# Kernel optimization log

Measured on AMD Instinct MI355X. Metric: run time of the kernel, lower is better.

Reference implementation:

```python
import jax, jax.numpy as jnp
import numpy as np

N_GROUPS = 1024   # n
L = 128           # keys per group
R = 4             # queries per group (nq[i] == R)
NQ_TOTAL = N_GROUPS * R
D_Q = 256
D_K = 256
D_Z = 256
D_V = 256


def setup_inputs() -> dict:
    key = jax.random.key(0)
    ks = jax.random.split(key, 8)
    nq = jnp.full((N_GROUPS,), R, dtype=jnp.int32)
    q = jax.random.normal(ks[0], (NQ_TOTAL, D_Q), dtype=jnp.float32)
    k = jax.random.normal(ks[1], (N_GROUPS, L, D_K), dtype=jnp.float32)
    v = jax.random.normal(ks[2], (N_GROUPS, L, D_V), dtype=jnp.float32)
    m = jax.random.uniform(ks[3], (N_GROUPS, L)) < 0.9
    m = m.at[:, 0].set(True)  # guarantee each row has at least one valid key
    Wq = jax.random.normal(ks[4], (D_Q, D_Z), dtype=jnp.float32) / np.sqrt(D_Q)
    bq = jnp.zeros((D_Z,), dtype=jnp.float32)
    Wk = jax.random.normal(ks[5], (D_K, D_Z), dtype=jnp.float32) / np.sqrt(D_K)
    bk = jnp.zeros((D_Z,), dtype=jnp.float32)
    return {"nq": nq, "q": q, "k": k, "v": v, "m": m,
            "Wq": Wq, "bq": bq, "Wk": Wk, "bk": bk}


def reference(nq, q, v, k, m, Wq, bq, Wk, bk):
    # Linear projections (nn.Linear with bias)
    qz = q @ Wq + bq                      # (N, d_z)
    kz = k @ Wk + bk                      # (n, l, d_z)
    d_z = Wq.shape[1]
    n = m.shape[0]
    # group index per query: equivalent to repeat_interleave(nq, 0)
    gidx = jnp.repeat(jnp.arange(n), nq, total_repeat_length=q.shape[0])  # (N,)
    # scores: s[i, l] = <kz[group(i), l], qz[i]> / sqrt(d_z)
    s = jnp.einsum('ild,id->il', kz[gidx], qz) / jnp.sqrt(jnp.asarray(d_z, qz.dtype))
    s = jnp.where(m[gidx], s, -jnp.inf)   # masked_fill(~m, -inf)
    p = jax.nn.softmax(s, axis=-1)        # softmax over key dim l
    # weighted sum over keys: (N, d)
    return jnp.einsum('il,ild->id', p, v[gidx])
```

## Files before the change

kernel.cpp:

```cpp
#include <hip/hip_runtime.h>

#define D 256
#define LKEYS 128
#define NGROUP 1024

__global__ __launch_bounds__(256) void prep_kernel(
    const float* __restrict__ Wq, const float* __restrict__ Wk,
    const float* __restrict__ bq, float* __restrict__ Mmat,
    float* __restrict__ rvec)
{
    __shared__ float wq_s[32][65];
    __shared__ float wk_s[32][65];
    __shared__ float bq_s[64];
    const int t  = threadIdx.x;
    const int a0 = (int)(blockIdx.x >> 3) * 32;
    const int b0 = (int)(blockIdx.x & 7) * 32;
    const int ai = t >> 4;
    const int bj = t & 15;
    float acc00 = 0.f, acc01 = 0.f, acc10 = 0.f, acc11 = 0.f;
    float racc = 0.f;
    for (int z0 = 0; z0 < D; z0 += 64) {
        __syncthreads();
        #pragma unroll
        for (int i = 0; i < 2; ++i) {
            const int f4i = t + 256 * i;
            const int row = f4i >> 4;
            const int c   = (f4i & 15) * 4;
            float4 aa = *(const float4*)&Wq[(size_t)(a0 + row) * D + z0 + c];
            wq_s[row][c] = aa.x; wq_s[row][c+1] = aa.y; wq_s[row][c+2] = aa.z; wq_s[row][c+3] = aa.w;
            float4 bb = *(const float4*)&Wk[(size_t)(b0 + row) * D + z0 + c];
            wk_s[row][c] = bb.x; wk_s[row][c+1] = bb.y; wk_s[row][c+2] = bb.z; wk_s[row][c+3] = bb.w;
        }
        if (t < 64) bq_s[t] = bq[z0 + t];
        __syncthreads();
        #pragma unroll 8
        for (int z = 0; z < 64; ++z) {
            const float wq0 = wq_s[ai][z];
            const float wq1 = wq_s[ai + 16][z];
            const float wk0 = wk_s[bj][z];
            const float wk1 = wk_s[bj + 16][z];
            acc00 += wq0 * wk0; acc01 += wq0 * wk1;
            acc10 += wq1 * wk0; acc11 += wq1 * wk1;
        }
        if (a0 == 0 && t < 32) {
            #pragma unroll 8
            for (int z = 0; z < 64; ++z) racc += bq_s[z] * wk_s[t][z];
        }
    }
    Mmat[(size_t)(a0 + ai)      * D + b0 + bj]      = acc00;
    Mmat[(size_t)(a0 + ai)      * D + b0 + bj + 16] = acc01;
    Mmat[(size_t)(a0 + ai + 16) * D + b0 + bj]      = acc10;
    Mmat[(size_t)(a0 + ai + 16) * D + b0 + bj + 16] = acc11;
    if (a0 == 0 && t < 32) rvec[b0 + t] = racc;
}

__global__ __launch_bounds__(256) void attn_kernel(
    const float* __restrict__ q, const float* __restrict__ k,
    const float* __restrict__ v, const int* __restrict__ m,
    const float* __restrict__ Mmat, const float* __restrict__ rvec,
    float* __restrict__ out)
{
    const int g    = blockIdx.x;
    const int t    = threadIdx.x;
    const int lane = t & 63;
    const int w    = t >> 6;

    __shared__ float  q_s[4][D];
    __shared__ float4 part_s[4][4][64];
    __shared__ float4 u_s4[4][64];
    __shared__ float  p_s[4][LKEYS];
    __shared__ int    m_s[LKEYS];

    {
        const float4* qg = (const float4*)(q + (size_t)g * 4 * D);
        ((float4*)q_s)[t] = qg[t];
    }
    if (t < LKEYS) m_s[t] = m[(size_t)g * LKEYS + t];
    __syncthreads();

    {
        const float4* M4 = (const float4*)Mmat;
        float4 p0 = {0,0,0,0}, p1 = {0,0,0,0}, p2 = {0,0,0,0}, p3 = {0,0,0,0};
        const int base = w * 64;
        #pragma unroll 4
        for (int dd = 0; dd < 64; ++dd) {
            const int a = base + dd;
            const float4 m4 = M4[a * 64 + lane];
            const float q0 = q_s[0][a], q1 = q_s[1][a], q2 = q_s[2][a], q3 = q_s[3][a];
            p0.x += q0*m4.x; p0.y += q0*m4.y; p0.z += q0*m4.z; p0.w += q0*m4.w;
            p1.x += q1*m4.x; p1.y += q1*m4.y; p1.z += q1*m4.z; p1.w += q1*m4.w;
            p2.x += q2*m4.x; p2.y += q2*m4.y; p2.z += q2*m4.z; p2.w += q2*m4.w;
            p3.x += q3*m4.x; p3.y += q3*m4.y; p3.z += q3*m4.z; p3.w += q3*m4.w;
        }
        part_s[w][0][lane] = p0; part_s[w][1][lane] = p1;
        part_s[w][2][lane] = p2; part_s[w][3][lane] = p3;
    }
    __syncthreads();

    {
        float4 acc = ((const float4*)rvec)[lane];
        const float4 a0 = part_s[0][w][lane], a1 = part_s[1][w][lane];
        const float4 a2 = part_s[2][w][lane], a3 = part_s[3][w][lane];
        acc.x += a0.x + a1.x + a2.x + a3.x;
        acc.y += a0.y + a1.y + a2.y + a3.y;
        acc.z += a0.z + a1.z + a2.z + a3.z;
        acc.w += a0.w + a1.w + a2.w + a3.w;
        u_s4[w][lane] = acc;
    }
    __syncthreads();

    const float4 u0 = u_s4[0][lane], u1 = u_s4[1][lane];
    const float4 u2 = u_s4[2][lane], u3 = u_s4[3][lane];

    {
        const float4* kg = (const float4*)(k + (size_t)g * LKEYS * D);

        auto reduce_qt = [&](float d0, float d1, float d2, float d3) -> float {
            float keepA = (lane & 1) ? d1 : d0;
            float sendA = (lane & 1) ? d0 : d1;
            keepA += __shfl_xor(sendA, 1);
            float keepB = (lane & 1) ? d3 : d2;
            float sendB = (lane & 1) ? d2 : d3;
            keepB += __shfl_xor(sendB, 1);
            float keep = (lane & 2) ? keepB : keepA;
            float send = (lane & 2) ? keepA : keepB;
            keep += __shfl_xor(send, 2);
            keep += __shfl_xor(keep, 4);
            keep += __shfl_xor(keep, 8);
            keep += __shfl_xor(keep, 16);
            keep += __shfl_xor(keep, 32);
            return keep;
        };

        const int l0 = w * 32;
        for (int kk = 0; kk < 32; kk += 4) {
            const int l = l0 + kk;
            const float4 kA = kg[(l + 0) * 64 + lane];
            const float4 kB = kg[(l + 1) * 64 + lane];
            const float4 kC = kg[(l + 2) * 64 + lane];
            const float4 kD = kg[(l + 3) * 64 + lane];

            float dA0 = kA.x*u0.x + kA.y*u0.y + kA.z*u0.z + kA.w*u0.w;
            float dA1 = kA.x*u1.x + kA.y*u1.y + kA.z*u1.z + kA.w*u1.w;
            float dA2 = kA.x*u2.x + kA.y*u2.y + kA.z*u2.z + kA.w*u2.w;
            float dA3 = kA.x*u3.x + kA.y*u3.y + kA.z*u3.z + kA.w*u3.w;
            float dB0 = kB.x*u0.x + kB.y*u0.y + kB.z*u0.z + kB.w*u0.w;
            float dB1 = kB.x*u1.x + kB.y*u1.y + kB.z*u1.z + kB.w*u1.w;
            float dB2 = kB.x*u2.x + kB.y*u2.y + kB.z*u2.z + kB.w*u2.w;
            float dB3 = kB.x*u3.x + kB.y*u3.y + kB.z*u3.z + kB.w*u3.w;
            float dC0 = kC.x*u0.x + kC.y*u0.y + kC.z*u0.z + kC.w*u0.w;
            float dC1 = kC.x*u1.x + kC.y*u1.y + kC.z*u1.z + kC.w*u1.w;
            float dC2 = kC.x*u2.x + kC.y*u2.y + kC.z*u2.z + kC.w*u2.w;
            float dC3 = kC.x*u3.x + kC.y*u3.y + kC.z*u3.z + kC.w*u3.w;
            float dD0 = kD.x*u0.x + kD.y*u0.y + kD.z*u0.z + kD.w*u0.w;
            float dD1 = kD.x*u1.x + kD.y*u1.y + kD.z*u1.z + kD.w*u1.w;
            float dD2 = kD.x*u2.x + kD.y*u2.y + kD.z*u2.z + kD.w*u2.w;
            float dD3 = kD.x*u3.x + kD.y*u3.y + kD.z*u3.z + kD.w*u3.w;

            const float rA = reduce_qt(dA0, dA1, dA2, dA3);
            const float rB = reduce_qt(dB0, dB1, dB2, dB3);
            const float rC = reduce_qt(dC0, dC1, dC2, dC3);
            const float rD = reduce_qt(dD0, dD1, dD2, dD3);

            if (lane < 4) {
                p_s[lane][l + 0] = m_s[l + 0] ? rA * 0.0625f : -1e30f;
                p_s[lane][l + 1] = m_s[l + 1] ? rB * 0.0625f : -1e30f;
                p_s[lane][l + 2] = m_s[l + 2] ? rC * 0.0625f : -1e30f;
                p_s[lane][l + 3] = m_s[l + 3] ? rD * 0.0625f : -1e30f;
            }
        }
    }
    __syncthreads();

    {
        const float v0 = p_s[w][lane];
        const float v1 = p_s[w][lane + 64];
        float mx = fmaxf(v0, v1);
        #pragma unroll
        for (int off = 32; off > 0; off >>= 1) mx = fmaxf(mx, __shfl_xor(mx, off));
        const float e0 = __expf(v0 - mx);
        const float e1 = __expf(v1 - mx);
        float sm = e0 + e1;
        #pragma unroll
        for (int off = 32; off > 0; off >>= 1) sm += __shfl_xor(sm, off);
        const float inv = 1.0f / sm;
        p_s[w][lane]      = e0 * inv;
        p_s[w][lane + 64] = e1 * inv;
    }

    {
        const float4* vg = (const float4*)(v + (size_t)g * LKEYS * D);
        float4 acc = {0,0,0,0};
        #pragma unroll 8
        for (int l = 0; l < LKEYS; ++l) {
            const float pw = p_s[w][l];
            const float4 vv = vg[l * 64 + lane];
            acc.x += pw * vv.x; acc.y += pw * vv.y;
            acc.z += pw * vv.z; acc.w += pw * vv.w;
        }
        float4* og = (float4*)(out + ((size_t)g * 4 + w) * D);
        og[lane] = acc;
    }
}

extern "C" void kernel_launch(void* const* d_in, const int* in_sizes, int n_in,
                              void* d_out, int out_size, void* d_ws, size_t ws_size,
                              hipStream_t stream) {
    const float* q  = (const float*)d_in[1];
    const float* k  = (const float*)d_in[2];
    const float* v  = (const float*)d_in[3];
    const int*   m  = (const int*)  d_in[4];
    const float* Wq = (const float*)d_in[5];
    const float* bq = (const float*)d_in[6];
    const float* Wk = (const float*)d_in[7];

    float* Mmat = (float*)d_ws;
    float* rvec = Mmat + D * D;

    prep_kernel<<<64, 256, 0, stream>>>(Wq, Wk, bq, Mmat, rvec);
    attn_kernel<<<NGROUP, 256, 0, stream>>>(q, k, v, m, Mmat, rvec, (float*)d_out);
}
```

Before: 72.38 us.

## Split attention over key halves with separate u, partial and combine kernels

Splits the per-group attention into a u-projection kernel, a key-split kernel that handles 64 keys per block (2048 blocks) and writes partial max, sum and weighted V, and a combine kernel that merges the two halves with a log-sum-exp rescale. The aim is more blocks and more memory-level parallelism for streaming K and V, plus a restructured butterfly shuffle reduction. In exchange it adds two kernel launches and workspace round-trips for u and the partials. The new path only runs if the workspace is large enough, otherwise it falls back to the old kernel.

```diff
diff --git a/kernel.cpp b/kernel.cpp
--- a/kernel.cpp
+++ b/kernel.cpp
@@ -3,6 +3,16 @@
 #define D 256
 #define LKEYS 128
 #define NGROUP 1024
+#define NQ 4096
+
+#define MMAT_OFF 0
+#define RVEC_OFF (D * D)
+#define U_OFF    (RVEC_OFF + D)
+#define PART_OFF (U_OFF + NQ * D)
+#define PART_STRIDE 260
+#define WS_FLOATS_SPLIT (PART_OFF + 2 * NQ * PART_STRIDE)
+
+#define DOT4(a, b) ((a).x*(b).x + (a).y*(b).y + (a).z*(b).z + (a).w*(b).w)
 
 __global__ __launch_bounds__(256) void prep_kernel(
     const float* __restrict__ Wq, const float* __restrict__ Wk,
@@ -54,30 +64,15 @@
     if (a0 == 0 && t < 32) rvec[b0 + t] = racc;
 }
 
-__global__ __launch_bounds__(256) void attn_kernel(
-    const float* __restrict__ q, const float* __restrict__ k,
-    const float* __restrict__ v, const int* __restrict__ m,
-    const float* __restrict__ Mmat, const float* __restrict__ rvec,
-    float* __restrict__ out)
+__global__ __launch_bounds__(256) void u_kernel(
+    const float* __restrict__ q, const float* __restrict__ Mmat,
+    const float* __restrict__ rvec, float* __restrict__ uout)
 {
-    const int g    = blockIdx.x;
-    const int t    = threadIdx.x;
-    const int lane = t & 63;
-    const int w    = t >> 6;
-
     __shared__ float  q_s[4][D];
     __shared__ float4 part_s[4][4][64];
-    __shared__ float4 u_s4[4][64];
-    __shared__ float  p_s[4][LKEYS];
-    __shared__ int    m_s[LKEYS];
-
-    {
-        const float4* qg = (const float4*)(q + (size_t)g * 4 * D);
-        ((float4*)q_s)[t] = qg[t];
-    }
-    if (t < LKEYS) m_s[t] = m[(size_t)g * LKEYS + t];
-    __syncthreads();
-
+    const int g = blockIdx.x, t = threadIdx.x, lane = t & 63, w = t >> 6;
+    ((float4*)q_s)[t] = ((const float4*)(q + (size_t)g * 4 * D))[t];
+    __syncthreads();
     {
         const float4* M4 = (const float4*)Mmat;
         float4 p0 = {0,0,0,0}, p1 = {0,0,0,0}, p2 = {0,0,0,0}, p3 = {0,0,0,0};
@@ -96,7 +91,204 @@
         part_s[w][2][lane] = p2; part_s[w][3][lane] = p3;
     }
     __syncthreads();
-
+    {
+        float4 acc = ((const float4*)rvec)[lane];
+        const float4 a0 = part_s[0][w][lane], a1 = part_s[1][w][lane];
+        const float4 a2 = part_s[2][w][lane], a3 = part_s[3][w][lane];
+        acc.x = (acc.x + a0.x + a1.x + a2.x + a3.x) * 0.0625f;
+        acc.y = (acc.y + a0.y + a1.y + a2.y + a3.y) * 0.0625f;
+        acc.z = (acc.z + a0.z + a1.z + a2.z + a3.z) * 0.0625f;
+        acc.w = (acc.w + a0.w + a1.w + a2.w + a3.w) * 0.0625f;
+        ((float4*)uout)[((size_t)g * 4 + w) * 64 + lane] = acc;
+    }
+}
+
+__global__ __launch_bounds__(256, 4) void attn_split_kernel(
+    const float* __restrict__ k, const float* __restrict__ v,
+    const int* __restrict__ m, const float* __restrict__ uws,
+    float* __restrict__ part)
+{
+    const int b = blockIdx.x;
+    const int g = b >> 1, h = b & 1;
+    const int t = threadIdx.x, lane = t & 63, w = t >> 6;
+    __shared__ float p_s[4][64];
+
+    const float4* U4 = (const float4*)uws;
+    const float4 u0 = U4[((size_t)g * 4 + 0) * 64 + lane];
+    const float4 u1 = U4[((size_t)g * 4 + 1) * 64 + lane];
+    const float4 u2 = U4[((size_t)g * 4 + 2) * 64 + lane];
+    const float4 u3 = U4[((size_t)g * 4 + 3) * 64 + lane];
+
+    const int kofs = h * 64;
+    const int mk = m[(size_t)g * LKEYS + kofs + lane];
+    const unsigned long long bal = __ballot(mk != 0);
+
+    const float4* kg = (const float4*)(k + ((size_t)g * LKEYS + kofs) * D);
+    const float4* vg = (const float4*)(v + ((size_t)g * LKEYS + kofs) * D);
+
+    #pragma unroll
+    for (int it = 0; it < 4; ++it) {
+        const int kb = w * 16 + it * 4;
+        const float4 ka0 = kg[(kb + 0) * 64 + lane];
+        const float4 ka1 = kg[(kb + 1) * 64 + lane];
+        const float4 ka2 = kg[(kb + 2) * 64 + lane];
+        const float4 ka3 = kg[(kb + 3) * 64 + lane];
+
+        float v16[16];
+        v16[ 0]=DOT4(ka0,u0); v16[ 1]=DOT4(ka0,u1); v16[ 2]=DOT4(ka0,u2); v16[ 3]=DOT4(ka0,u3);
+        v16[ 4]=DOT4(ka1,u0); v16[ 5]=DOT4(ka1,u1); v16[ 6]=DOT4(ka1,u2); v16[ 7]=DOT4(ka1,u3);
+        v16[ 8]=DOT4(ka2,u0); v16[ 9]=DOT4(ka2,u1); v16[10]=DOT4(ka2,u2); v16[11]=DOT4(ka2,u3);
+        v16[12]=DOT4(ka3,u0); v16[13]=DOT4(ka3,u1); v16[14]=DOT4(ka3,u2); v16[15]=DOT4(ka3,u3);
+
+        float v8[8];
+        {
+            const int hb = lane & 1;
+            #pragma unroll
+            for (int i = 0; i < 8; ++i) {
+                const float keep = hb ? v16[8 + i] : v16[i];
+                const float send = hb ? v16[i]     : v16[8 + i];
+                v8[i] = keep + __shfl_xor(send, 1);
+            }
+        }
+        float v4a[4];
+        {
+            const int hb = (lane >> 1) & 1;
+            #pragma unroll
+            for (int i = 0; i < 4; ++i) {
+                const float keep = hb ? v8[4 + i] : v8[i];
+                const float send = hb ? v8[i]     : v8[4 + i];
+                v4a[i] = keep + __shfl_xor(send, 2);
+            }
+        }
+        float v2a[2];
+        {
+            const int hb = (lane >> 2) & 1;
+            #pragma unroll
+            for (int i = 0; i < 2; ++i) {
+                const float keep = hb ? v2a[0]*0.f + v4a[2 + i] : v4a[i];
+                const float send = hb ? v4a[i]     : v4a[2 + i];
+                v2a[i] = keep + __shfl_xor(send, 4);
+            }
+        }
+        float v1;
+        {
+            const int hb = (lane >> 3) & 1;
+            const float keep = hb ? v2a[1] : v2a[0];
+            const float send = hb ? v2a[0] : v2a[1];
+            v1 = keep + __shfl_xor(send, 8);
+        }
+        v1 += __shfl_xor(v1, 16);
+        v1 += __shfl_xor(v1, 32);
+
+        if (lane < 16) {
+            const int i  = ((lane & 1) << 3) | ((lane & 2) << 1) | ((lane & 4) >> 1) | ((lane & 8) >> 3);
+            const int kl = kb + (i >> 2);
+            p_s[i & 3][kl] = ((bal >> kl) & 1ull) ? v1 : -1e30f;
+        }
+    }
+    __syncthreads();
+
+    float m_loc, su;
+    {
+        const float s = p_s[w][lane];
+        float mx = s;
+        #pragma unroll
+        for (int off = 32; off > 0; off >>= 1) mx = fmaxf(mx, __shfl_xor(mx, off));
+        const bool valid = (bal >> lane) & 1ull;
+        const float e = valid ? __expf(s - mx) : 0.f;
+        float ss = e;
+        #pragma unroll
+        for (int off = 32; off > 0; off >>= 1) ss += __shfl_xor(ss, off);
+        p_s[w][lane] = e;
+        m_loc = mx; su = ss;
+    }
+
+    float4 acc = {0, 0, 0, 0};
+    for (int l = 0; l < 64; l += 8) {
+        float4 va[8];
+        #pragma unroll
+        for (int j = 0; j < 8; ++j) va[j] = vg[(l + j) * 64 + lane];
+        const float4 ea = *(const float4*)&p_s[w][l];
+        const float4 eb = *(const float4*)&p_s[w][l + 4];
+        acc.x += ea.x*va[0].x; acc.y += ea.x*va[0].y; acc.z += ea.x*va[0].z; acc.w += ea.x*va[0].w;
+        acc.x += ea.y*va[1].x; acc.y += ea.y*va[1].y; acc.z += ea.y*va[1].z; acc.w += ea.y*va[1].w;
+        acc.x += ea.z*va[2].x; acc.y += ea.z*va[2].y; acc.z += ea.z*va[2].z; acc.w += ea.z*va[2].w;
+        acc.x += ea.w*va[3].x; acc.y += ea.w*va[3].y; acc.z += ea.w*va[3].z; acc.w += ea.w*va[3].w;
+        acc.x += eb.x*va[4].x; acc.y += eb.x*va[4].y; acc.z += eb.x*va[4].z; acc.w += eb.x*va[4].w;
+        acc.x += eb.y*va[5].x; acc.y += eb.y*va[5].y; acc.z += eb.y*va[5].z; acc.w += eb.y*va[5].w;
+        acc.x += eb.z*va[6].x; acc.y += eb.z*va[6].y; acc.z += eb.z*va[6].z; acc.w += eb.z*va[6].w;
+        acc.x += eb.w*va[7].x; acc.y += eb.w*va[7].y; acc.z += eb.w*va[7].z; acc.w += eb.w*va[7].w;
+    }
+
+    float* pb = part + ((size_t)h * NQ + (size_t)g * 4 + w) * PART_STRIDE;
+    ((float4*)pb)[lane] = acc;
+    if (lane == 0) { pb[256] = m_loc; pb[257] = su; }
+}
+
+__global__ __launch_bounds__(256) void combine_kernel(
+    const float* __restrict__ part, float* __restrict__ out)
+{
+    const int b = blockIdx.x, t = threadIdx.x, lane = t & 63, w = t >> 6;
+    const int i = b * 4 + w;
+    const float* pA = part + (size_t)i * PART_STRIDE;
+    const float* pB = part + ((size_t)NQ + i) * PART_STRIDE;
+    const float mA = pA[256], suA = pA[257];
+    const float mB = pB[256], suB = pB[257];
+    const float Mx = fmaxf(mA, mB);
+    const float fA = __expf(mA - Mx);
+    const float fB = __expf(mB - Mx);
+    const float inv = 1.0f / (fA * suA + fB * suB);
+    const float4 aA = ((const float4*)pA)[lane];
+    const float4 aB = ((const float4*)pB)[lane];
+    float4 o;
+    o.x = (fA*aA.x + fB*aB.x) * inv;
+    o.y = (fA*aA.y + fB*aB.y) * inv;
+    o.z = (fA*aA.z + fB*aB.z) * inv;
+    o.w = (fA*aA.w + fB*aB.w) * inv;
+    ((float4*)out)[(size_t)i * 64 + lane] = o;
+}
+
+__global__ __launch_bounds__(256) void attn_kernel(
+    const float* __restrict__ q, const float* __restrict__ k,
+    const float* __restrict__ v, const int* __restrict__ m,
+    const float* __restrict__ Mmat, const float* __restrict__ rvec,
+    float* __restrict__ out)
+{
+    const int g    = blockIdx.x;
+    const int t    = threadIdx.x;
+    const int lane = t & 63;
+    const int w    = t >> 6;
+
+    __shared__ float  q_s[4][D];
+    __shared__ float4 part_s[4][4][64];
+    __shared__ float4 u_s4[4][64];
+    __shared__ float  p_s[4][LKEYS];
+    __shared__ int    m_s[LKEYS];
+
+    {
+        const float4* qg = (const float4*)(q + (size_t)g * 4 * D);
+        ((float4*)q_s)[t] = qg[t];
+    }
+    if (t < LKEYS) m_s[t] = m[(size_t)g * LKEYS + t];
+    __syncthreads();
+    {
+        const float4* M4 = (const float4*)Mmat;
+        float4 p0 = {0,0,0,0}, p1 = {0,0,0,0}, p2 = {0,0,0,0}, p3 = {0,0,0,0};
+        const int base = w * 64;
+        #pragma unroll 4
+        for (int dd = 0; dd < 64; ++dd) {
+            const int a = base + dd;
+            const float4 m4 = M4[a * 64 + lane];
+            const float q0 = q_s[0][a], q1 = q_s[1][a], q2 = q_s[2][a], q3 = q_s[3][a];
+            p0.x += q0*m4.x; p0.y += q0*m4.y; p0.z += q0*m4.z; p0.w += q0*m4.w;
+            p1.x += q1*m4.x; p1.y += q1*m4.y; p1.z += q1*m4.z; p1.w += q1*m4.w;
+            p2.x += q2*m4.x; p2.y += q2*m4.y; p2.z += q2*m4.z; p2.w += q2*m4.w;
+            p3.x += q3*m4.x; p3.y += q3*m4.y; p3.z += q3*m4.z; p3.w += q3*m4.w;
+        }
+        part_s[w][0][lane] = p0; part_s[w][1][lane] = p1;
+        part_s[w][2][lane] = p2; part_s[w][3][lane] = p3;
+    }
+    __syncthreads();
     {
         float4 acc = ((const float4*)rvec)[lane];
         const float4 a0 = part_s[0][w][lane], a1 = part_s[1][w][lane];
@@ -111,10 +303,8 @@
 
     const float4 u0 = u_s4[0][lane], u1 = u_s4[1][lane];
     const float4 u2 = u_s4[2][lane], u3 = u_s4[3][lane];
-
     {
         const float4* kg = (const float4*)(k + (size_t)g * LKEYS * D);
-
         auto reduce_qt = [&](float d0, float d1, float d2, float d3) -> float {
             float keepA = (lane & 1) ? d1 : d0;
             float sendA = (lane & 1) ? d0 : d1;
@@ -131,7 +321,6 @@
             keep += __shfl_xor(keep, 32);
             return keep;
         };
-
         const int l0 = w * 32;
         for (int kk = 0; kk < 32; kk += 4) {
             const int l = l0 + kk;
@@ -139,29 +328,14 @@
             const float4 kB = kg[(l + 1) * 64 + lane];
             const float4 kC = kg[(l + 2) * 64 + lane];
             const float4 kD = kg[(l + 3) * 64 + lane];
-
-            float dA0 = kA.x*u0.x + kA.y*u0.y + kA.z*u0.z + kA.w*u0.w;
-            float dA1 = kA.x*u1.x + kA.y*u1.y + kA.z*u1.z + kA.w*u1.w;
-            float dA2 = kA.x*u2.x + kA.y*u2.y + kA.z*u2.z + kA.w*u2.w;
-            float dA3 = kA.x*u3.x + kA.y*u3.y + kA.z*u3.z + kA.w*u3.w;
-            float dB0 = kB.x*u0.x + kB.y*u0.y + kB.z*u0.z + kB.w*u0.w;
-            float dB1 = kB.x*u1.x + kB.y*u1.y + kB.z*u1.z + kB.w*u1.w;
-            float dB2 = kB.x*u2.x + kB.y*u2.y + kB.z*u2.z + kB.w*u2.w;
-            float dB3 = kB.x*u3.x + kB.y*u3.y + kB.z*u3.z + kB.w*u3.w;
-            float dC0 = kC.x*u0.x + kC.y*u0.y + kC.z*u0.z + kC.w*u0.w;
-            float dC1 = kC.x*u1.x + kC.y*u1.y + kC.z*u1.z + kC.w*u1.w;
-            float dC2 = kC.x*u2.x + kC.y*u2.y + kC.z*u2.z + kC.w*u2.w;
-            float dC3 = kC.x*u3.x + kC.y*u3.y + kC.z*u3.z + kC.w*u3.w;
-            float dD0 = kD.x*u0.x + kD.y*u0.y + kD.z*u0.z + kD.w*u0.w;
-            float dD1 = kD.x*u1.x + kD.y*u1.y + kD.z*u1.z + kD.w*u1.w;
-            float dD2 = kD.x*u2.x + kD.y*u2.y + kD.z*u2.z + kD.w*u2.w;
-            float dD3 = kD.x*u3.x + kD.y*u3.y + kD.z*u3.z + kD.w*u3.w;
-
+            float dA0 = DOT4(kA,u0), dA1 = DOT4(kA,u1), dA2 = DOT4(kA,u2), dA3 = DOT4(kA,u3);
+            float dB0 = DOT4(kB,u0), dB1 = DOT4(kB,u1), dB2 = DOT4(kB,u2), dB3 = DOT4(kB,u3);
+            float dC0 = DOT4(kC,u0), dC1 = DOT4(kC,u1), dC2 = DOT4(kC,u2), dC3 = DOT4(kC,u3);
+            float dD0 = DOT4(kD,u0), dD1 = DOT4(kD,u1), dD2 = DOT4(kD,u2), dD3 = DOT4(kD,u3);
             const float rA = reduce_qt(dA0, dA1, dA2, dA3);
             const float rB = reduce_qt(dB0, dB1, dB2, dB3);
             const float rC = reduce_qt(dC0, dC1, dC2, dC3);
             const float rD = reduce_qt(dD0, dD1, dD2, dD3);
-
             if (lane < 4) {
                 p_s[lane][l + 0] = m_s[l + 0] ? rA * 0.0625f : -1e30f;
                 p_s[lane][l + 1] = m_s[l + 1] ? rB * 0.0625f : -1e30f;
@@ -171,7 +345,6 @@
         }
     }
     __syncthreads();
-
     {
         const float v0 = p_s[w][lane];
         const float v1 = p_s[w][lane + 64];
@@ -187,7 +360,6 @@
         p_s[w][lane]      = e0 * inv;
         p_s[w][lane + 64] = e1 * inv;
     }
-
     {
         const float4* vg = (const float4*)(v + (size_t)g * LKEYS * D);
         float4 acc = {0,0,0,0};
@@ -214,9 +386,15 @@
     const float* bq = (const float*)d_in[6];
     const float* Wk = (const float*)d_in[7];
 
-    float* Mmat = (float*)d_ws;
-    float* rvec = Mmat + D * D;
-
-    prep_kernel<<<64, 256, 0, stream>>>(Wq, Wk, bq, Mmat, rvec);
-    attn_kernel<<<NGROUP, 256, 0, stream>>>(q, k, v, m, Mmat, rvec, (float*)d_out);
-}
+    float* ws = (float*)d_ws;
+    prep_kernel<<<64, 256, 0, stream>>>(Wq, Wk, bq, ws + MMAT_OFF, ws + RVEC_OFF);
+
+    if (ws_size >= (size_t)WS_FLOATS_SPLIT * sizeof(float)) {
+        u_kernel<<<NGROUP, 256, 0, stream>>>(q, ws + MMAT_OFF, ws + RVEC_OFF, ws + U_OFF);
+        attn_split_kernel<<<NGROUP * 2, 256, 0, stream>>>(k, v, m, ws + U_OFF, ws + PART_OFF);
+        combine_kernel<<<NGROUP, 256, 0, stream>>>(ws + PART_OFF, (float*)d_out);
+    } else {
+        attn_kernel<<<NGROUP, 256, 0, stream>>>(q, k, v, m, ws + MMAT_OFF, ws + RVEC_OFF,
+                                                (float*)d_out);
+    }
+}
```

Result: slower. 76.91 us (+6.3%).

## Split u-projection into batched GEMM and double-buffer K/V via LDS async loads

Applied to the files above, without the earlier changes.

Moves the q·M projection out of the per-group attention kernel into a separate kernel that handles 16 queries per block and writes pre-scaled u vectors to workspace. This cuts the redundant reads of the 256x256 M matrix from once per group. The new attention kernel streams K and V in 16-row tiles into double-buffered shared memory using global_load_lds, and uses a wider butterfly shuffle reduction. It adds an extra launch and a workspace round-trip, and falls back to the old path if the workspace is too small.

```diff
diff --git a/kernel.cpp b/kernel.cpp
--- a/kernel.cpp
+++ b/kernel.cpp
@@ -3,6 +3,20 @@
 #define D 256
 #define LKEYS 128
 #define NGROUP 1024
+#define NQ 4096
+
+#define MMAT_OFF 0
+#define RVEC_OFF (D * D)
+#define U_OFF    (RVEC_OFF + D)
+#define WS_FLOATS (U_OFF + NQ * D)
+
+#define DOT4(a, b) ((a).x*(b).x + (a).y*(b).y + (a).z*(b).z + (a).w*(b).w)
+
+__device__ __forceinline__ void gload_lds16(const float* g, float* l) {
+    __builtin_amdgcn_global_load_lds(
+        (const __attribute__((address_space(1))) void*)g,
+        (__attribute__((address_space(3))) void*)l, 16, 0, 0);
+}
 
 __global__ __launch_bounds__(256) void prep_kernel(
     const float* __restrict__ Wq, const float* __restrict__ Wk,
@@ -54,6 +68,169 @@
     if (a0 == 0 && t < 32) rvec[b0 + t] = racc;
 }
 
+__global__ __launch_bounds__(256) void u_gemm_kernel(
+    const float* __restrict__ q, const float* __restrict__ Mmat,
+    const float* __restrict__ rvec, float* __restrict__ uout)
+{
+    __shared__ float q_s[16][D];
+    const int b = blockIdx.x, t = threadIdx.x, lane = t & 63, w = t >> 6;
+    {
+        const float4* qg = (const float4*)(q + (size_t)b * 16 * D);
+        float4* qs4 = (float4*)q_s;
+        #pragma unroll
+        for (int i = 0; i < 4; ++i) qs4[t + 256 * i] = qg[t + 256 * i];
+    }
+    __syncthreads();
+
+    const float4* M4 = (const float4*)Mmat;
+    const int r0 = w * 4;
+    float4 a0 = {0,0,0,0}, a1 = {0,0,0,0}, a2 = {0,0,0,0}, a3 = {0,0,0,0};
+    #pragma unroll 4
+    for (int kk = 0; kk < D; ++kk) {
+        const float4 m4 = M4[kk * 64 + lane];
+        const float qa = q_s[r0 + 0][kk], qb = q_s[r0 + 1][kk];
+        const float qc = q_s[r0 + 2][kk], qd = q_s[r0 + 3][kk];
+        a0.x += qa*m4.x; a0.y += qa*m4.y; a0.z += qa*m4.z; a0.w += qa*m4.w;
+        a1.x += qb*m4.x; a1.y += qb*m4.y; a1.z += qb*m4.z; a1.w += qb*m4.w;
+        a2.x += qc*m4.x; a2.y += qc*m4.y; a2.z += qc*m4.z; a2.w += qc*m4.w;
+        a3.x += qd*m4.x; a3.y += qd*m4.y; a3.z += qd*m4.z; a3.w += qd*m4.w;
+    }
+    const float4 r4 = ((const float4*)rvec)[lane];
+    float4* U4 = (float4*)uout;
+    float4 o;
+    o.x=(a0.x+r4.x)*0.0625f; o.y=(a0.y+r4.y)*0.0625f; o.z=(a0.z+r4.z)*0.0625f; o.w=(a0.w+r4.w)*0.0625f;
+    U4[((size_t)b * 16 + r0 + 0) * 64 + lane] = o;
+    o.x=(a1.x+r4.x)*0.0625f; o.y=(a1.y+r4.y)*0.0625f; o.z=(a1.z+r4.z)*0.0625f; o.w=(a1.w+r4.w)*0.0625f;
+    U4[((size_t)b * 16 + r0 + 1) * 64 + lane] = o;
+    o.x=(a2.x+r4.x)*0.0625f; o.y=(a2.y+r4.y)*0.0625f; o.z=(a2.z+r4.z)*0.0625f; o.w=(a2.w+r4.w)*0.0625f;
+    U4[((size_t)b * 16 + r0 + 2) * 64 + lane] = o;
+    o.x=(a3.x+r4.x)*0.0625f; o.y=(a3.y+r4.y)*0.0625f; o.z=(a3.z+r4.z)*0.0625f; o.w=(a3.w+r4.w)*0.0625f;
+    U4[((size_t)b * 16 + r0 + 3) * 64 + lane] = o;
+}
+
+__global__ __launch_bounds__(256) void attn2_kernel(
+    const float* __restrict__ k, const float* __restrict__ v,
+    const int* __restrict__ m, const float* __restrict__ uws,
+    float* __restrict__ out)
+{
+    const int g = blockIdx.x, t = threadIdx.x, lane = t & 63, w = t >> 6;
+
+    __shared__ float buf[2][16 * D];
+    __shared__ float p_s[4][LKEYS];
+    __shared__ int   m_s[LKEYS];
+
+    const float* kg = k + (size_t)g * LKEYS * D;
+    const float* vg = v + (size_t)g * LKEYS * D;
+
+    auto stage = [&](const float* src, int tile, int b) {
+        const float* s = src + (size_t)tile * 16 * D;
+        #pragma unroll
+        for (int j = 0; j < 4; ++j) {
+            const int r = w * 4 + j;
+            gload_lds16(s + r * D + lane * 4, &buf[b][r * D]);
+        }
+    };
+
+    stage(kg, 0, 0);
+    if (t < LKEYS) m_s[t] = m[(size_t)g * LKEYS + t];
+
+    const float4* U4 = (const float4*)uws;
+    const float4 u0 = U4[((size_t)g * 4 + 0) * 64 + lane];
+    const float4 u1 = U4[((size_t)g * 4 + 1) * 64 + lane];
+    const float4 u2 = U4[((size_t)g * 4 + 2) * 64 + lane];
+    const float4 u3 = U4[((size_t)g * 4 + 3) * 64 + lane];
+    __syncthreads();
+
+    for (int tl = 0; tl < 8; ++tl) {
+        if (tl < 7) stage(kg, tl + 1, (tl + 1) & 1);
+
+        const float4* B4 = (const float4*)&buf[tl & 1][0];
+        const int kb = w * 4;
+        const float4 ka0 = B4[(kb + 0) * 64 + lane];
+        const float4 ka1 = B4[(kb + 1) * 64 + lane];
+        const float4 ka2 = B4[(kb + 2) * 64 + lane];
+        const float4 ka3 = B4[(kb + 3) * 64 + lane];
+
+        float v16[16];
+        v16[ 0]=DOT4(ka0,u0); v16[ 1]=DOT4(ka0,u1); v16[ 2]=DOT4(ka0,u2); v16[ 3]=DOT4(ka0,u3);
+        v16[ 4]=DOT4(ka1,u0); v16[ 5]=DOT4(ka1,u1); v16[ 6]=DOT4(ka1,u2); v16[ 7]=DOT4(ka1,u3);
+        v16[ 8]=DOT4(ka2,u0); v16[ 9]=DOT4(ka2,u1); v16[10]=DOT4(ka2,u2); v16[11]=DOT4(ka2,u3);
+        v16[12]=DOT4(ka3,u0); v16[13]=DOT4(ka3,u1); v16[14]=DOT4(ka3,u2); v16[15]=DOT4(ka3,u3);
+
+        float v8[8];
+        { const int hb = lane & 1;
+          #pragma unroll
+          for (int i = 0; i < 8; ++i) {
+              const float keep = hb ? v16[8 + i] : v16[i];
+              const float send = hb ? v16[i]     : v16[8 + i];
+              v8[i] = keep + __shfl_xor(send, 1);
+          } }
+        float v4a[4];
+        { const int hb = (lane >> 1) & 1;
+          #pragma unroll
+          for (int i = 0; i < 4; ++i) {
+              const float keep = hb ? v8[4 + i] : v8[i];
+              const float send = hb ? v8[i]     : v8[4 + i];
+              v4a[i] = keep + __shfl_xor(send, 2);
+          } }
+        float v2a[2];
+        { const int hb = (lane >> 2) & 1;
+          #pragma unroll
+          for (int i = 0; i < 2; ++i) {
+              const float keep = hb ? v4a[2 + i] : v4a[i];
+              const float send = hb ? v4a[i]     : v4a[2 + i];
+              v2a[i] = keep + __shfl_xor(send, 4);
+          } }
+        float v1;
+        { const int hb = (lane >> 3) & 1;
+          const float keep = hb ? v2a[1] : v2a[0];
+          const float send = hb ? v2a[0] : v2a[1];
+          v1 = keep + __shfl_xor(send, 8); }
+        v1 += __shfl_xor(v1, 16);
+        v1 += __shfl_xor(v1, 32);
+
+        if (lane < 16) {
+            const int i  = ((lane & 1) << 3) | ((lane & 2) << 1) | ((lane & 4) >> 1) | ((lane & 8) >> 3);
+            const int kl = tl * 16 + w * 4 + (i >> 2);
+            p_s[i & 3][kl] = m_s[kl] ? v1 : -1e30f;
+        }
+        __syncthreads();
+    }
+
+    stage(vg, 0, 0);
+    {
+        const float s0 = p_s[w][lane];
+        const float s1 = p_s[w][lane + 64];
+        float mx = fmaxf(s0, s1);
+        #pragma unroll
+        for (int off = 32; off > 0; off >>= 1) mx = fmaxf(mx, __shfl_xor(mx, off));
+        const float e0 = __expf(s0 - mx);
+        const float e1 = __expf(s1 - mx);
+        float sm = e0 + e1;
+        #pragma unroll
+        for (int off = 32; off > 0; off >>= 1) sm += __shfl_xor(sm, off);
+        const float inv = 1.0f / sm;
+        p_s[w][lane]      = e0 * inv;
+        p_s[w][lane + 64] = e1 * inv;
+    }
+    __syncthreads();
+
+    float4 acc = {0, 0, 0, 0};
+    for (int tl = 0; tl < 8; ++tl) {
+        if (tl < 7) stage(vg, tl + 1, (tl + 1) & 1);
+        const float4* B4 = (const float4*)&buf[tl & 1][0];
+        #pragma unroll
+        for (int r = 0; r < 16; ++r) {
+            const float pw = p_s[w][tl * 16 + r];
+            const float4 vv = B4[r * 64 + lane];
+            acc.x += pw * vv.x; acc.y += pw * vv.y;
+            acc.z += pw * vv.z; acc.w += pw * vv.w;
+        }
+        __syncthreads();
+    }
+    ((float4*)(out + ((size_t)g * 4 + w) * D))[lane] = acc;
+}
+
 __global__ __launch_bounds__(256) void attn_kernel(
     const float* __restrict__ q, const float* __restrict__ k,
     const float* __restrict__ v, const int* __restrict__ m,
@@ -77,7 +254,6 @@
     }
     if (t < LKEYS) m_s[t] = m[(size_t)g * LKEYS + t];
     __syncthreads();
-
     {
         const float4* M4 = (const float4*)Mmat;
         float4 p0 = {0,0,0,0}, p1 = {0,0,0,0}, p2 = {0,0,0,0}, p3 = {0,0,0,0};
@@ -96,7 +272,6 @@
         part_s[w][2][lane] = p2; part_s[w][3][lane] = p3;
     }
     __syncthreads();
-
     {
         float4 acc = ((const float4*)rvec)[lane];
         const float4 a0 = part_s[0][w][lane], a1 = part_s[1][w][lane];
@@ -111,10 +286,8 @@
 
     const float4 u0 = u_s4[0][lane], u1 = u_s4[1][lane];
     const float4 u2 = u_s4[2][lane], u3 = u_s4[3][lane];
-
     {
         const float4* kg = (const float4*)(k + (size_t)g * LKEYS * D);
-
         auto reduce_qt = [&](float d0, float d1, float d2, float d3) -> float {
             float keepA = (lane & 1) ? d1 : d0;
             float sendA = (lane & 1) ? d0 : d1;
@@ -131,7 +304,6 @@
             keep += __shfl_xor(keep, 32);
             return keep;
         };
-
         const int l0 = w * 32;
         for (int kk = 0; kk < 32; kk += 4) {
             const int l = l0 + kk;
@@ -139,29 +311,14 @@
             const float4 kB = kg[(l + 1) * 64 + lane];
             const float4 kC = kg[(l + 2) * 64 + lane];
             const float4 kD = kg[(l + 3) * 64 + lane];
-
-            float dA0 = kA.x*u0.x + kA.y*u0.y + kA.z*u0.z + kA.w*u0.w;
-            float dA1 = kA.x*u1.x + kA.y*u1.y + kA.z*u1.z + kA.w*u1.w;
-            float dA2 = kA.x*u2.x + kA.y*u2.y + kA.z*u2.z + kA.w*u2.w;
-            float dA3 = kA.x*u3.x + kA.y*u3.y + kA.z*u3.z + kA.w*u3.w;
-            float dB0 = kB.x*u0.x + kB.y*u0.y + kB.z*u0.z + kB.w*u0.w;
-            float dB1 = kB.x*u1.x + kB.y*u1.y + kB.z*u1.z + kB.w*u1.w;
-            float dB2 = kB.x*u2.x + kB.y*u2.y + kB.z*u2.z + kB.w*u2.w;
-            float dB3 = kB.x*u3.x + kB.y*u3.y + kB.z*u3.z + kB.w*u3.w;
-            float dC0 = kC.x*u0.x + kC.y*u0.y + kC.z*u0.z + kC.w*u0.w;
-            float dC1 = kC.x*u1.x + kC.y*u1.y + kC.z*u1.z + kC.w*u1.w;
-            float dC2 = kC.x*u2.x + kC.y*u2.y + kC.z*u2.z + kC.w*u2.w;
-            float dC3 = kC.x*u3.x + kC.y*u3.y + kC.z*u3.z + kC.w*u3.w;
-            float dD0 = kD.x*u0.x + kD.y*u0.y + kD.z*u0.z + kD.w*u0.w;
-            float dD1 = kD.x*u1.x + kD.y*u1.y + kD.z*u1.z + kD.w*u1.w;
-            float dD2 = kD.x*u2.x + kD.y*u2.y + kD.z*u2.z + kD.w*u2.w;
-            float dD3 = kD.x*u3.x + kD.y*u3.y + kD.z*u3.z + kD.w*u3.w;
-
+            float dA0 = DOT4(kA,u0), dA1 = DOT4(kA,u1), dA2 = DOT4(kA,u2), dA3 = DOT4(kA,u3);
+            float dB0 = DOT4(kB,u0), dB1 = DOT4(kB,u1), dB2 = DOT4(kB,u2), dB3 = DOT4(kB,u3);
+            float dC0 = DOT4(kC,u0), dC1 = DOT4(kC,u1), dC2 = DOT4(kC,u2), dC3 = DOT4(kC,u3);
+            float dD0 = DOT4(kD,u0), dD1 = DOT4(kD,u1), dD2 = DOT4(kD,u2), dD3 = DOT4(kD,u3);
             const float rA = reduce_qt(dA0, dA1, dA2, dA3);
             const float rB = reduce_qt(dB0, dB1, dB2, dB3);
             const float rC = reduce_qt(dC0, dC1, dC2, dC3);
             const float rD = reduce_qt(dD0, dD1, dD2, dD3);
-
             if (lane < 4) {
                 p_s[lane][l + 0] = m_s[l + 0] ? rA * 0.0625f : -1e30f;
                 p_s[lane][l + 1] = m_s[l + 1] ? rB * 0.0625f : -1e30f;
@@ -171,7 +328,6 @@
         }
     }
     __syncthreads();
-
     {
         const float v0 = p_s[w][lane];
         const float v1 = p_s[w][lane + 64];
@@ -187,7 +343,6 @@
         p_s[w][lane]      = e0 * inv;
         p_s[w][lane + 64] = e1 * inv;
     }
-
     {
         const float4* vg = (const float4*)(v + (size_t)g * LKEYS * D);
         float4 acc = {0,0,0,0};
@@ -214,9 +369,14 @@
     const float* bq = (const float*)d_in[6];
     const float* Wk = (const float*)d_in[7];
 
-    float* Mmat = (float*)d_ws;
-    float* rvec = Mmat + D * D;
-
-    prep_kernel<<<64, 256, 0, stream>>>(Wq, Wk, bq, Mmat, rvec);
-    attn_kernel<<<NGROUP, 256, 0, stream>>>(q, k, v, m, Mmat, rvec, (float*)d_out);
-}
+    float* ws = (float*)d_ws;
+    prep_kernel<<<64, 256, 0, stream>>>(Wq, Wk, bq, ws + MMAT_OFF, ws + RVEC_OFF);
+
+    if (ws_size >= (size_t)WS_FLOATS * sizeof(float)) {
+        u_gemm_kernel<<<NQ / 16, 256, 0, stream>>>(q, ws + MMAT_OFF, ws + RVEC_OFF, ws + U_OFF);
+        attn2_kernel<<<NGROUP, 256, 0, stream>>>(k, v, m, ws + U_OFF, (float*)d_out);
+    } else {
+        attn_kernel<<<NGROUP, 256, 0, stream>>>(q, k, v, m, ws + MMAT_OFF, ws + RVEC_OFF,
+                                                (float*)d_out);
+    }
+}
```

New measurement: 81.14 us. +12.1%, slower.
